# Kernel optimization log

Measured on AMD Instinct MI355X. Metric: run time of the kernel, lower is better.

The kernel has to match this reference:

```python
import jax, jax.numpy as jnp
import numpy as np

N, E, G = 50000, 600000, 256
IN_C, EMB, HID, OUT = 64, 128, 128, 36


def _glorot(key, fan_in, fan_out):
    lim = np.sqrt(6.0 / (fan_in + fan_out)).astype(np.float32)
    return jax.random.uniform(key, (fan_in, fan_out), jnp.float32, -lim, lim)


def setup_inputs() -> dict:
    key = jax.random.key(0)
    ks = jax.random.split(key, 12)
    x = jax.random.normal(ks[0], (N, IN_C), jnp.float32)
    edge_index = jax.random.randint(ks[1], (2, E), 0, N, jnp.int64)
    edge_attr = jax.random.uniform(ks[2], (E,), jnp.float32)
    # deterministic sorted batch assignment -> every graph id 0..G-1 is nonempty
    batch = ((jnp.arange(N, dtype=jnp.int64) * G) // N).astype(jnp.int64)
    rho = jax.random.uniform(ks[3], (G,), jnp.float32)
    return {
        "x": x,
        "edge_attr": edge_attr,
        "rho": rho,
        "conv0_w": _glorot(ks[4], IN_C, EMB),
        "conv0_b": jnp.zeros((EMB,), jnp.float32),
        "conv1_w": _glorot(ks[5], EMB, EMB),
        "conv1_b": jnp.zeros((EMB,), jnp.float32),
        "mlp0_w": _glorot(ks[6], 2 * EMB + 1, HID),
        "mlp0_b": jnp.zeros((HID,), jnp.float32),
        "mlp1_w": _glorot(ks[7], HID, HID),
        "mlp1_b": jnp.zeros((HID,), jnp.float32),
        "out_w": _glorot(ks[8], HID, OUT),
        "out_b": jnp.zeros((OUT,), jnp.float32),
        "edge_index": edge_index,
        "batch": batch,
    }


def _gcn_conv(h, row, col, w, W, b):
    # PyG GCNConv: self-loops already appended in (row, col, w).
    deg = jax.ops.segment_sum(w, col, num_segments=N)  # in-degree by edge weight
    dis = jnp.where(deg > 0, jax.lax.rsqrt(jnp.maximum(deg, 1e-30)), 0.0)
    norm = dis[row] * w * dis[col]                     # [E+N]
    h = h @ W                                          # [N, out]
    msg = norm[:, None] * h[row]                       # gather + scale
    return jax.ops.segment_sum(msg, col, num_segments=N) + b


def reference(x, edge_attr, rho, conv0_w, conv0_b, conv1_w, conv1_b,
              mlp0_w, mlp0_b, mlp1_w, mlp1_b, out_w, out_b,
              edge_index, batch):
    # add self-loops with weight 1
    loops = jnp.arange(N, dtype=edge_index.dtype)
    row = jnp.concatenate([edge_index[0], loops])
    col = jnp.concatenate([edge_index[1], loops])
    w = jnp.concatenate([edge_attr, jnp.ones((N,), edge_attr.dtype)])

    h = jax.nn.relu(_gcn_conv(x, row, col, w, conv0_w, conv0_b))
    h = jax.nn.relu(_gcn_conv(h, row, col, w, conv1_w, conv1_b))

    gmp = jax.ops.segment_max(h, batch, num_segments=G)             # [G, EMB]
    cnt = jax.ops.segment_sum(jnp.ones((N,), h.dtype), batch, num_segments=G)
    gap = jax.ops.segment_sum(h, batch, num_segments=G) / cnt[:, None]
    hg = jnp.concatenate([gmp, gap, rho[:, None]], axis=1)          # [G, 2*EMB+1]

    hg = jax.nn.relu(hg @ mlp0_w + mlp0_b)
    hg = jax.nn.relu(hg @ mlp1_w + mlp1_b)
    return hg @ out_w + out_b
```

## Files before the change

### kernel.cpp

```cpp
#include <hip/hip_runtime.h>
#include <hip/hip_fp16.h>
#include <math.h>

using half8 = __attribute__((ext_vector_type(8))) _Float16;
using f32x4 = __attribute__((ext_vector_type(4))) float;

#define CAP 64


__device__ __forceinline__ float wdec(unsigned int v) {
    __half h;
    *reinterpret_cast<unsigned short*>(&h) = (unsigned short)(v >> 16);
    return __half2float(h);
}

__device__ __forceinline__ unsigned int wenc(int src, float w) {
    __half h = __float2half(w);
    return (unsigned int)src |
           ((unsigned int)(*reinterpret_cast<unsigned short*>(&h)) << 16);
}

__device__ __forceinline__ float4 ld_half4(const __half* p) {
    int2 raw = *reinterpret_cast<const int2*>(p);
    __half2 a = *reinterpret_cast<__half2*>(&raw.x);
    __half2 b = *reinterpret_cast<__half2*>(&raw.y);
    return make_float4(__low2float(a), __high2float(a), __low2float(b), __high2float(b));
}

__device__ __forceinline__ void st_half4(__half* p, float4 v) {
    __half2 a = __floats2half2_rn(v.x, v.y);
    __half2 b = __floats2half2_rn(v.z, v.w);
    int2 raw;
    raw.x = *reinterpret_cast<int*>(&a);
    raw.y = *reinterpret_cast<int*>(&b);
    *reinterpret_cast<int2*>(p) = raw;
}


__global__ void k_setup(const float* __restrict__ w0, __half* __restrict__ wt0,
                        const float* __restrict__ w1, __half* __restrict__ wt1,
                        int* __restrict__ cursor, int n) {
    int i = blockIdx.x * blockDim.x + threadIdx.x;
    if (i < 64 * 128) {
        int k = i >> 7, c = i & 127;
        wt0[c * 64 + k] = __float2half(w0[i]);
    }
    if (i < 128 * 128) {
        int k = i >> 7, c = i & 127;
        wt1[c * 128 + k] = __float2half(w1[i]);
    }
    if (i < n) cursor[i] = 0;
}


__global__ void k_place(const int* __restrict__ row, const int* __restrict__ col,
                        const float* __restrict__ w, int* __restrict__ cursor,
                        unsigned int* __restrict__ slab, int e) {
    int i = blockIdx.x * blockDim.x + threadIdx.x;
    if (i < e) {
        int c = col[i];
        int s = atomicAdd(&cursor[c], 1);
        if (s < CAP) slab[(size_t)c * CAP + s] = wenc(row[i], w[i]);
    }
}

__global__ __launch_bounds__(256) void k_degscale(
    const unsigned int* __restrict__ slab, const int* __restrict__ cursor,
    const float* __restrict__ x, float* __restrict__ dis,
    __half* __restrict__ xs, int n)
{
    __shared__ float sdis[256];
    int t = threadIdx.x;
    int base = blockIdx.x * 256;
    int i = base + t;
    if (i < n) {
        int cnt = min(cursor[i], CAP);
        float s = 1.0f;
        const unsigned int* p = &slab[(size_t)i * CAP];
        int j = 0;
        for (; j + 4 <= cnt; j += 4) {
            uint4 rec = *reinterpret_cast<const uint4*>(&p[j]);
            s += wdec(rec.x) + wdec(rec.y) + wdec(rec.z) + wdec(rec.w);
        }
        for (; j < cnt; ++j) s += wdec(p[j]);
        float d = rsqrtf(s);
        dis[i] = d;
        sdis[t] = d;
    }
    __syncthreads();
#pragma unroll
    for (int it = 0; it < 16; ++it) {
        int id = it * 256 + t;
        int node_l = id >> 4;
        if (base + node_l < n) {
            float d = sdis[node_l];
            float4 v = reinterpret_cast<const float4*>(x)[(size_t)base * 16 + id];
            v.x *= d; v.y *= d; v.z *= d; v.w *= d;
            st_half4(&xs[((size_t)base * 16 + id) * 4], v);
        }
    }
}


template<int COLS, int LPN>
__global__ __launch_bounds__(256) void k_agg(
    const __half* __restrict__ hs, const unsigned int* __restrict__ slab,
    const int* __restrict__ cursor, const float* __restrict__ dis,
    __half* __restrict__ out, int n)
{
    int t = blockIdx.x * blockDim.x + threadIdx.x;
    int node = t / LPN, lane = t % LPN;
    if (node >= n) return;
    int c4 = lane * 4;
    float4 acc = ld_half4(&hs[(size_t)node * COLS + c4]);
    int cnt = min(cursor[node], CAP);
    const unsigned int* sp = &slab[(size_t)node * CAP];
    int p = 0;
    for (; p + 4 <= cnt; p += 4) {
        uint4 rec = *reinterpret_cast<const uint4*>(&sp[p]);
        float w0 = wdec(rec.x), w1 = wdec(rec.y), w2 = wdec(rec.z), w3 = wdec(rec.w);
        float4 v0 = ld_half4(&hs[(size_t)(rec.x & 0xFFFF) * COLS + c4]);
        float4 v1 = ld_half4(&hs[(size_t)(rec.y & 0xFFFF) * COLS + c4]);
        float4 v2 = ld_half4(&hs[(size_t)(rec.z & 0xFFFF) * COLS + c4]);
        float4 v3 = ld_half4(&hs[(size_t)(rec.w & 0xFFFF) * COLS + c4]);
        acc.x = fmaf(w0, v0.x, acc.x); acc.y = fmaf(w0, v0.y, acc.y);
        acc.z = fmaf(w0, v0.z, acc.z); acc.w = fmaf(w0, v0.w, acc.w);
        acc.x = fmaf(w1, v1.x, acc.x); acc.y = fmaf(w1, v1.y, acc.y);
        acc.z = fmaf(w1, v1.z, acc.z); acc.w = fmaf(w1, v1.w, acc.w);
        acc.x = fmaf(w2, v2.x, acc.x); acc.y = fmaf(w2, v2.y, acc.y);
        acc.z = fmaf(w2, v2.z, acc.z); acc.w = fmaf(w2, v2.w, acc.w);
        acc.x = fmaf(w3, v3.x, acc.x); acc.y = fmaf(w3, v3.y, acc.y);
        acc.z = fmaf(w3, v3.z, acc.z); acc.w = fmaf(w3, v3.w, acc.w);
    }
    for (; p < cnt; ++p) {
        unsigned int rec = sp[p];
        float w0 = wdec(rec);
        float4 v0 = ld_half4(&hs[(size_t)(rec & 0xFFFF) * COLS + c4]);
        acc.x = fmaf(w0, v0.x, acc.x); acc.y = fmaf(w0, v0.y, acc.y);
        acc.z = fmaf(w0, v0.z, acc.z); acc.w = fmaf(w0, v0.w, acc.w);
    }
    float d = dis[node];
    float4 o;
    o.x = d * acc.x; o.y = d * acc.y; o.z = d * acc.z; o.w = d * acc.w;
    st_half4(&out[(size_t)node * COLS + c4], o);
}


template<int K, bool SC>
__global__ __launch_bounds__(256) void k_gemm_mfma(
    const __half* __restrict__ A, const __half* __restrict__ wt,
    const float* __restrict__ bias, const float* __restrict__ scale,
    __half* __restrict__ out, int n)
{
    constexpr int SA = K + 8;
    constexpr int CPR = K / 8;
    __shared__ _Float16 Al[64 * SA];
    __shared__ _Float16 Wl[128 * SA];
    const int tid = threadIdx.x;
    const int row0 = blockIdx.x * 64;

#pragma unroll
    for (int it = 0; it < (64 * CPR) / 256; ++it) {
        int id = tid + it * 256;
        int r = id / CPR, kc = id % CPR;
        int gr = row0 + r; if (gr >= n) gr = n - 1;
        int4 raw = *reinterpret_cast<const int4*>(&A[(size_t)gr * K + kc * 8]);
        *reinterpret_cast<int4*>(&Al[r * SA + kc * 8]) = raw;
    }
#pragma unroll
    for (int it = 0; it < (128 * CPR) / 256; ++it) {
        int id = tid + it * 256;
        int c = id / CPR, kc = id % CPR;
        int4 raw = *reinterpret_cast<const int4*>(&wt[(size_t)c * K + kc * 8]);
        *reinterpret_cast<int4*>(&Wl[c * SA + kc * 8]) = raw;
    }
    __syncthreads();

    const int l = tid & 63, w = tid >> 6;
    const int r = l & 15, kg = l >> 4;

    f32x4 acc[8];
#pragma unroll
    for (int ct = 0; ct < 8; ++ct) acc[ct] = (f32x4){0.f, 0.f, 0.f, 0.f};

#pragma unroll
    for (int kst = 0; kst < K / 32; ++kst) {
        half8 af = *reinterpret_cast<const half8*>(&Al[(16 * w + r) * SA + kst * 32 + kg * 8]);
#pragma unroll
        for (int ct = 0; ct < 8; ++ct) {
            half8 bf = *reinterpret_cast<const half8*>(&Wl[(16 * ct + r) * SA + kst * 32 + kg * 8]);
            acc[ct] = __builtin_amdgcn_mfma_f32_16x16x32_f16(af, bf, acc[ct], 0, 0, 0);
        }
    }

    float sc[4];
#pragma unroll
    for (int q = 0; q < 4; ++q) {
        int gr = row0 + 16 * w + kg * 4 + q;
        sc[q] = (SC && gr < n) ? scale[gr] : 1.0f;
    }
#pragma unroll
    for (int ct = 0; ct < 8; ++ct) {
        float bv = bias[16 * ct + r];
#pragma unroll
        for (int q = 0; q < 4; ++q) {
            int gr = row0 + 16 * w + kg * 4 + q;
            if (gr < n) {
                float v = fmaxf(acc[ct][q] + bv, 0.f);
                if constexpr (SC) v *= sc[q];
                out[(size_t)gr * 128 + 16 * ct + r] = __float2half(v);
            }
        }
    }
}


__device__ __forceinline__ int lowbound(const int* __restrict__ b, int n, int key) {
    int lo = 0, hi = n;
    while (lo < hi) { int mid = (lo + hi) >> 1; if (b[mid] < key) lo = mid + 1; else hi = mid; }
    return lo;
}

#define NSLICE 8

__global__ __launch_bounds__(128) void k_pool_part(
    const __half* __restrict__ h, const int* __restrict__ batch,
    float* __restrict__ part, int n)
{
    int g = blockIdx.x >> 3, s = blockIdx.x & (NSLICE - 1);
    int ch = threadIdx.x;
    __shared__ int sbeg, send;
    if (ch == 0) {
        sbeg = lowbound(batch, n, g);
        send = lowbound(batch, n, g + 1);
    }
    __syncthreads();
    float mx = -INFINITY, sm = 0.f;
    for (int i = sbeg + s; i < send; i += NSLICE) {
        float v = __half2float(h[(size_t)i * 128 + ch]);
        mx = fmaxf(mx, v);
        sm += v;
    }
    size_t base = ((size_t)g * NSLICE + s) * 256;
    part[base + ch] = mx;
    part[base + 128 + ch] = sm;
}


__global__ __launch_bounds__(256) void k_head_mlp(
    const float* __restrict__ part, const int* __restrict__ batch,
    const float* __restrict__ rho,
    const float* __restrict__ w0, const float* __restrict__ b0,
    const float* __restrict__ w1, const float* __restrict__ b1,
    const float* __restrict__ w2, const float* __restrict__ b2,
    float* __restrict__ out, int n)
{
    int g = blockIdx.x;
    int tid = threadIdx.x;
    int ch = tid & 127, half = tid >> 7;
    __shared__ float hg[257];
    __shared__ float t0[128];
    __shared__ float red[2][128];
    __shared__ int scnt;
    if (tid == 0) {
        int beg = lowbound(batch, n, g);
        int end = lowbound(batch, n, g + 1);
        scnt = end - beg;
        hg[256] = rho[g];
    }
    {
        float mx = -INFINITY, sm = 0.f;
        for (int s = half * (NSLICE / 2); s < (half + 1) * (NSLICE / 2); ++s) {
            size_t base = ((size_t)g * NSLICE + s) * 256;
            mx = fmaxf(mx, part[base + ch]);
            sm += part[base + 128 + ch];
        }
        red[half][ch] = mx;
        __syncthreads();
        if (half == 0) {
            float m2 = fmaxf(mx, red[1][ch]);
            hg[ch] = m2;
            red[0][ch] = sm;
        }
        __syncthreads();
        if (half == 1) red[1][ch] = sm + red[0][ch];
        __syncthreads();
        if (half == 0) hg[128 + ch] = red[1][ch] / (float)scnt;
        __syncthreads();
    }
    {
        float a = 0.f, b = 0.f;
        int j0 = half * 128;
        int jend = half ? 257 : 128;
        int j = j0;
        for (; j + 2 <= jend; j += 2) {
            a = fmaf(hg[j], w0[(size_t)j * 128 + ch], a);
            b = fmaf(hg[j + 1], w0[(size_t)(j + 1) * 128 + ch], b);
        }
        if (j < jend) a = fmaf(hg[j], w0[(size_t)j * 128 + ch], a);
        red[half][ch] = a + b;
        __syncthreads();
        if (half == 0) t0[ch] = fmaxf(red[0][ch] + red[1][ch] + b0[ch], 0.f);
        __syncthreads();
    }
    {
        float a = 0.f, b = 0.f;
        int j0 = half * 64;
        for (int j = j0; j < j0 + 64; j += 2) {
            a = fmaf(t0[j], w1[(size_t)j * 128 + ch], a);
            b = fmaf(t0[j + 1], w1[(size_t)(j + 1) * 128 + ch], b);
        }
        red[half][ch] = a + b;
        __syncthreads();
        if (half == 0) hg[ch] = fmaxf(red[0][ch] + red[1][ch] + b1[ch], 0.f);
        __syncthreads();
    }
    if (ch < 36) {
        float a = 0.f, b = 0.f;
        int j0 = half * 64;
        for (int j = j0; j < j0 + 64; j += 2) {
            a = fmaf(hg[j], w2[(size_t)j * 36 + ch], a);
            b = fmaf(hg[j + 1], w2[(size_t)(j + 1) * 36 + ch], b);
        }
        red[half][ch] = a + b;
    }
    __syncthreads();
    if (half == 0 && ch < 36)
        out[(size_t)g * 36 + ch] = red[0][ch] + red[1][ch] + b2[ch];
}


extern "C" void kernel_launch(void* const* d_in, const int* in_sizes, int n_in,
                              void* d_out, int out_size, void* d_ws, size_t ws_size,
                              hipStream_t stream)
{
    const float* x        = (const float*)d_in[0];
    const float* edge_attr= (const float*)d_in[1];
    const float* rho      = (const float*)d_in[2];
    const float* conv0_w  = (const float*)d_in[3];
    const float* conv0_b  = (const float*)d_in[4];
    const float* conv1_w  = (const float*)d_in[5];
    const float* conv1_b  = (const float*)d_in[6];
    const float* mlp0_w   = (const float*)d_in[7];
    const float* mlp0_b   = (const float*)d_in[8];
    const float* mlp1_w   = (const float*)d_in[9];
    const float* mlp1_b   = (const float*)d_in[10];
    const float* out_w    = (const float*)d_in[11];
    const float* out_b    = (const float*)d_in[12];
    const int*   edge_idx = (const int*)d_in[13];
    const int*   batch    = (const int*)d_in[14];

    const int N = in_sizes[0] / 64;
    const int E = in_sizes[1];
    const int G = in_sizes[2];
    const int* erow = edge_idx;
    const int* ecol = edge_idx + E;

    char* ws = (char*)d_ws;
    size_t off = 0;
    auto alloc = [&](size_t bytes) -> void* {
        off = (off + 255) & ~(size_t)255;
        void* p = ws + off;
        off += bytes;
        return p;
    };
    float*        dis    = (float*)alloc((size_t)N * 4);
    int*          cursor = (int*)  alloc((size_t)N * 4);
    unsigned int* slab   = (unsigned int*)alloc((size_t)N * CAP * 4);
    __half*       bufA   = (__half*)alloc((size_t)N * 128 * 2);
    __half*       bufB   = (__half*)alloc((size_t)N * 128 * 2);
    float*        part   = (float*)alloc((size_t)G * NSLICE * 256 * 4);
    __half*       wt0    = (__half*)alloc((size_t)64 * 128 * 2);
    __half*       wt1    = (__half*)alloc((size_t)128 * 128 * 2);

    dim3 b256(256);
    int setup_n = (N > 128 * 128) ? N : 128 * 128;
    k_setup<<<(setup_n + 255) / 256, b256, 0, stream>>>(conv0_w, wt0, conv1_w, wt1, cursor, N);
    k_place<<<(E + 255) / 256, b256, 0, stream>>>(erow, ecol, edge_attr, cursor, slab, E);
    k_degscale<<<(N + 255) / 256, b256, 0, stream>>>(slab, cursor, x, dis, bufA, N);

    k_agg<64, 16><<<((size_t)N * 16 + 255) / 256, b256, 0, stream>>>(bufA, slab, cursor, dis, bufB, N);
    k_gemm_mfma<64, true><<<(N + 63) / 64, b256, 0, stream>>>(bufB, wt0, conv0_b, dis, bufA, N);
    k_agg<128, 32><<<((size_t)N * 32 + 255) / 256, b256, 0, stream>>>(bufA, slab, cursor, dis, bufB, N);
    k_gemm_mfma<128, false><<<(N + 63) / 64, b256, 0, stream>>>(bufB, wt1, conv1_b, nullptr, bufA, N);

    k_pool_part<<<G * NSLICE, dim3(128), 0, stream>>>(bufA, batch, part, N);
    k_head_mlp<<<G, b256, 0, stream>>>(part, batch, rho,
                                       mlp0_w, mlp0_b, mlp1_w, mlp1_b, out_w, out_b,
                                       (float*)d_out, N);
}
```

Baseline: 162.3 us.

## Fuse graph max/mean pooling into second GEMM epilogue via atomics

The per-graph max and sum pooling moves into the epilogue of the second MFMA GEMM. Each 64-row tile accumulates partial max/sum for at most two graphs, reduces them across lanes and waves, and commits them with float atomicMax (valid through int reinterpretation because values are non-negative after ReLU) and atomicAdd. This drops the separate pooling kernel and its re-read of the hidden features. The cost is extra registers and atomics in the GEMM, and the code assumes every 64-row tile spans at most two graphs, which holds here because each graph has about 195 nodes.

```diff
diff --git a/kernel.cpp b/kernel.cpp
--- a/kernel.cpp
+++ b/kernel.cpp
@@ -39,7 +39,8 @@
 
 __global__ void k_setup(const float* __restrict__ w0, __half* __restrict__ wt0,
                         const float* __restrict__ w1, __half* __restrict__ wt1,
-                        int* __restrict__ cursor, int n) {
+                        int* __restrict__ cursor, float* __restrict__ pmax,
+                        float* __restrict__ psum, int n, int gch) {
     int i = blockIdx.x * blockDim.x + threadIdx.x;
     if (i < 64 * 128) {
         int k = i >> 7, c = i & 127;
@@ -50,6 +51,7 @@
         wt1[c * 128 + k] = __float2half(w1[i]);
     }
     if (i < n) cursor[i] = 0;
+    if (i < gch) { pmax[i] = 0.f; psum[i] = 0.f; }
 }
 
 
@@ -146,11 +148,12 @@
 }
 
 
-template<int K, bool SC>
+template<int K, bool SC, bool POOL>
 __global__ __launch_bounds__(256) void k_gemm_mfma(
     const __half* __restrict__ A, const __half* __restrict__ wt,
     const float* __restrict__ bias, const float* __restrict__ scale,
-    __half* __restrict__ out, int n)
+    const int* __restrict__ batch, float* __restrict__ pmax,
+    float* __restrict__ psum, __half* __restrict__ out, int n)
 {
     constexpr int SA = K + 8;
     constexpr int CPR = K / 8;
@@ -194,10 +197,22 @@
     }
 
     float sc[4];
+    int bq[4];
+    int g0 = 0, g1 = 0;
+    if constexpr (POOL) {
+        g0 = batch[row0];
+        g1 = batch[(row0 + 63 < n) ? row0 + 63 : n - 1];
+    }
 #pragma unroll
     for (int q = 0; q < 4; ++q) {
         int gr = row0 + 16 * w + kg * 4 + q;
         sc[q] = (SC && gr < n) ? scale[gr] : 1.0f;
+        if constexpr (POOL) bq[q] = (gr < n) ? (batch[gr] - g0) : -1;
+    }
+    float pm0[8], ps0[8], pm1[8], ps1[8];
+    if constexpr (POOL) {
+#pragma unroll
+        for (int ct = 0; ct < 8; ++ct) { pm0[ct] = 0.f; ps0[ct] = 0.f; pm1[ct] = 0.f; ps1[ct] = 0.f; }
     }
 #pragma unroll
     for (int ct = 0; ct < 8; ++ct) {
@@ -209,7 +224,51 @@
                 float v = fmaxf(acc[ct][q] + bv, 0.f);
                 if constexpr (SC) v *= sc[q];
                 out[(size_t)gr * 128 + 16 * ct + r] = __float2half(v);
+                if constexpr (POOL) {
+                    if (bq[q] == 0) { pm0[ct] = fmaxf(pm0[ct], v); ps0[ct] += v; }
+                    else if (bq[q] == 1) { pm1[ct] = fmaxf(pm1[ct], v); ps1[ct] += v; }
+                }
             }
+        }
+    }
+
+    if constexpr (POOL) {
+#pragma unroll
+        for (int mask = 16; mask <= 32; mask <<= 1) {
+#pragma unroll
+            for (int ct = 0; ct < 8; ++ct) {
+                pm0[ct] = fmaxf(pm0[ct], __shfl_xor(pm0[ct], mask));
+                ps0[ct] += __shfl_xor(ps0[ct], mask);
+                pm1[ct] = fmaxf(pm1[ct], __shfl_xor(pm1[ct], mask));
+                ps1[ct] += __shfl_xor(ps1[ct], mask);
+            }
+        }
+        __syncthreads();
+        float* ldsm = reinterpret_cast<float*>(Wl);
+        float* ldss = ldsm + 4 * 2 * 128;
+        if (kg == 0) {
+#pragma unroll
+            for (int ct = 0; ct < 8; ++ct) {
+                int ch = 16 * ct + r;
+                ldsm[(w * 2 + 0) * 128 + ch] = pm0[ct];
+                ldsm[(w * 2 + 1) * 128 + ch] = pm1[ct];
+                ldss[(w * 2 + 0) * 128 + ch] = ps0[ct];
+                ldss[(w * 2 + 1) * 128 + ch] = ps1[ct];
+            }
+        }
+        __syncthreads();
+        int gslot = tid >> 7, ch = tid & 127;
+        bool valid = (gslot == 0) || (g1 != g0);
+        if (valid) {
+            float M = 0.f, S = 0.f;
+#pragma unroll
+            for (int ww = 0; ww < 4; ++ww) {
+                M = fmaxf(M, ldsm[(ww * 2 + gslot) * 128 + ch]);
+                S += ldss[(ww * 2 + gslot) * 128 + ch];
+            }
+            int g = g0 + gslot;
+            atomicMax(reinterpret_cast<int*>(&pmax[(size_t)g * 128 + ch]), __float_as_int(M));
+            atomicAdd(&psum[(size_t)g * 128 + ch], S);
         }
     }
 }
@@ -221,35 +280,9 @@
     return lo;
 }
 
-#define NSLICE 8
-
-__global__ __launch_bounds__(128) void k_pool_part(
-    const __half* __restrict__ h, const int* __restrict__ batch,
-    float* __restrict__ part, int n)
-{
-    int g = blockIdx.x >> 3, s = blockIdx.x & (NSLICE - 1);
-    int ch = threadIdx.x;
-    __shared__ int sbeg, send;
-    if (ch == 0) {
-        sbeg = lowbound(batch, n, g);
-        send = lowbound(batch, n, g + 1);
-    }
-    __syncthreads();
-    float mx = -INFINITY, sm = 0.f;
-    for (int i = sbeg + s; i < send; i += NSLICE) {
-        float v = __half2float(h[(size_t)i * 128 + ch]);
-        mx = fmaxf(mx, v);
-        sm += v;
-    }
-    size_t base = ((size_t)g * NSLICE + s) * 256;
-    part[base + ch] = mx;
-    part[base + 128 + ch] = sm;
-}
-
-
 __global__ __launch_bounds__(256) void k_head_mlp(
-    const float* __restrict__ part, const int* __restrict__ batch,
-    const float* __restrict__ rho,
+    const float* __restrict__ pmax, const float* __restrict__ psum,
+    const int* __restrict__ batch, const float* __restrict__ rho,
     const float* __restrict__ w0, const float* __restrict__ b0,
     const float* __restrict__ w1, const float* __restrict__ b1,
     const float* __restrict__ w2, const float* __restrict__ b2,
@@ -268,26 +301,12 @@
         scnt = end - beg;
         hg[256] = rho[g];
     }
-    {
-        float mx = -INFINITY, sm = 0.f;
-        for (int s = half * (NSLICE / 2); s < (half + 1) * (NSLICE / 2); ++s) {
-            size_t base = ((size_t)g * NSLICE + s) * 256;
-            mx = fmaxf(mx, part[base + ch]);
-            sm += part[base + 128 + ch];
-        }
-        red[half][ch] = mx;
-        __syncthreads();
-        if (half == 0) {
-            float m2 = fmaxf(mx, red[1][ch]);
-            hg[ch] = m2;
-            red[0][ch] = sm;
-        }
-        __syncthreads();
-        if (half == 1) red[1][ch] = sm + red[0][ch];
-        __syncthreads();
-        if (half == 0) hg[128 + ch] = red[1][ch] / (float)scnt;
-        __syncthreads();
-    }
+    __syncthreads();
+    if (half == 0) {
+        hg[ch] = pmax[(size_t)g * 128 + ch];
+        hg[128 + ch] = psum[(size_t)g * 128 + ch] / (float)scnt;
+    }
+    __syncthreads();
     {
         float a = 0.f, b = 0.f;
         int j0 = half * 128;
@@ -369,23 +388,29 @@
     unsigned int* slab   = (unsigned int*)alloc((size_t)N * CAP * 4);
     __half*       bufA   = (__half*)alloc((size_t)N * 128 * 2);
     __half*       bufB   = (__half*)alloc((size_t)N * 128 * 2);
-    float*        part   = (float*)alloc((size_t)G * NSLICE * 256 * 4);
+    float*        pmax   = (float*)alloc((size_t)G * 128 * 4);
+    float*        psum   = (float*)alloc((size_t)G * 128 * 4);
     __half*       wt0    = (__half*)alloc((size_t)64 * 128 * 2);
     __half*       wt1    = (__half*)alloc((size_t)128 * 128 * 2);
 
     dim3 b256(256);
-    int setup_n = (N > 128 * 128) ? N : 128 * 128;
-    k_setup<<<(setup_n + 255) / 256, b256, 0, stream>>>(conv0_w, wt0, conv1_w, wt1, cursor, N);
+    int gch = G * 128;
+    int setup_n = N;
+    if (setup_n < 128 * 128) setup_n = 128 * 128;
+    if (setup_n < gch) setup_n = gch;
+    k_setup<<<(setup_n + 255) / 256, b256, 0, stream>>>(conv0_w, wt0, conv1_w, wt1,
+                                                       cursor, pmax, psum, N, gch);
     k_place<<<(E + 255) / 256, b256, 0, stream>>>(erow, ecol, edge_attr, cursor, slab, E);
     k_degscale<<<(N + 255) / 256, b256, 0, stream>>>(slab, cursor, x, dis, bufA, N);
 
     k_agg<64, 16><<<((size_t)N * 16 + 255) / 256, b256, 0, stream>>>(bufA, slab, cursor, dis, bufB, N);
-    k_gemm_mfma<64, true><<<(N + 63) / 64, b256, 0, stream>>>(bufB, wt0, conv0_b, dis, bufA, N);
+    k_gemm_mfma<64, true, false><<<(N + 63) / 64, b256, 0, stream>>>(
+        bufB, wt0, conv0_b, dis, nullptr, nullptr, nullptr, bufA, N);
     k_agg<128, 32><<<((size_t)N * 32 + 255) / 256, b256, 0, stream>>>(bufA, slab, cursor, dis, bufB, N);
-    k_gemm_mfma<128, false><<<(N + 63) / 64, b256, 0, stream>>>(bufB, wt1, conv1_b, nullptr, bufA, N);
-
-    k_pool_part<<<G * NSLICE, dim3(128), 0, stream>>>(bufA, batch, part, N);
-    k_head_mlp<<<G, b256, 0, stream>>>(part, batch, rho,
+    k_gemm_mfma<128, false, true><<<(N + 63) / 64, b256, 0, stream>>>(
+        bufB, wt1, conv1_b, nullptr, batch, pmax, psum, bufA, N);
+
+    k_head_mlp<<<G, b256, 0, stream>>>(pmax, psum, batch, rho,
                                        mlp0_w, mlp0_b, mlp1_w, mlp1_b, out_w, out_b,
                                        (float*)d_out, N);
 }
```

Result: faster. 157.0 us (-3.3%).
